# Kernel tuning notes

Hardware: AMD Instinct MI355X
Metric: run time of the kernel (lower is better)

The kernel has to match this reference:

```python
import jax, jax.numpy as jnp
import numpy as np

N_NODES = 50000
N_EDGES = 800000
D_NODE = 128
D_EDGE = 16
HID = 128
BN_EPS = 1e-5


def gcn_conv(h, src, dst, W, b):
    # PyG GCNConv: h' = D^-1/2 (A + I) D^-1/2 (h W) + b, deg includes self-loop
    h = h @ W
    deg = jax.ops.segment_sum(jnp.ones((src.shape[0],), h.dtype), dst,
                              num_segments=N_NODES) + 1.0
    dinv = deg ** -0.5
    norm = dinv[src] * dinv[dst]                      # [E]
    agg = jax.ops.segment_sum(h[src] * norm[:, None], dst,
                              num_segments=N_NODES)   # scatter to dst
    agg = agg + h * (dinv * dinv)[:, None]            # self-loop term
    return agg + b


def setup_inputs() -> dict:
    key = jax.random.key(0)
    ks = jax.random.split(key, 12)
    s = lambda fan_in: 1.0 / np.sqrt(fan_in)
    return {
        "x": jax.random.normal(ks[0], (N_NODES, D_NODE), jnp.float32),
        "edge_index": jax.random.randint(ks[1], (2, N_EDGES), 0, N_NODES, jnp.int32),
        "edge_attr": jax.random.normal(ks[2], (N_EDGES, D_EDGE), jnp.float32),
        "W1": jax.random.normal(ks[3], (D_NODE, HID), jnp.float32) * s(D_NODE),
        "b1": jnp.zeros((HID,), jnp.float32),
        "gamma": jnp.ones((HID,), jnp.float32),
        "beta": jnp.zeros((HID,), jnp.float32),
        "W2": jax.random.normal(ks[4], (HID, HID), jnp.float32) * s(HID),
        "b2": jnp.zeros((HID,), jnp.float32),
        "Wm1": jax.random.normal(ks[5], (2 * HID + D_EDGE, HID), jnp.float32) * s(2 * HID + D_EDGE),
        "bm1": jnp.zeros((HID,), jnp.float32),
        "Wm2": jax.random.normal(ks[6], (HID, 1), jnp.float32) * s(HID),
        "bm2": jnp.zeros((1,), jnp.float32),
    }


def reference(x, edge_index, edge_attr, W1, b1, gamma, beta, W2, b2, Wm1, bm1, Wm2, bm2):
    src, dst = edge_index[0], edge_index[1]
    z = gcn_conv(x, src, dst, W1, b1)
    # BatchNorm1d over nodes (training-mode batch stats, biased var)
    mean = jnp.mean(z, axis=0)
    var = jnp.mean(jnp.square(z - mean), axis=0)
    z = (z - mean) * jax.lax.rsqrt(var + BN_EPS) * gamma + beta
    z = jax.nn.relu(z)
    z = gcn_conv(z, src, dst, W2, b2)
    # edge head: gather endpoints, concat with edge_attr, 2-layer MLP (dropout = eval identity)
    edge_input = jnp.concatenate([z[src], z[dst], edge_attr], axis=1)  # [E, 2H+De]
    h = jax.nn.relu(edge_input @ Wm1 + bm1)
    return (h @ Wm2 + bm2).squeeze(-1)  # [E]
```

## Files before the change

### kernel.cpp

```cpp
#include <hip/hip_runtime.h>
#include <hip/hip_bf16.h>

#define NN 50000
#define NE 800000
#define H 128
#define DE 16
#define BN_EPS 1e-5f
#define NB_SCAN 196
#define NB_E 3125

typedef float v2f __attribute__((ext_vector_type(2)));
typedef float v4f __attribute__((ext_vector_type(4)));
typedef short bfrag __attribute__((ext_vector_type(8)));

__device__ __forceinline__ unsigned int packbf2(float a, float b) {
    __hip_bfloat162 h = __float22bfloat162_rn(make_float2(a, b));
    return *(unsigned int*)&h;
}
__device__ __forceinline__ v2f unpackbf2(unsigned int u) {
    v2f r;
    r.x = __uint_as_float(u << 16);
    r.y = __uint_as_float(u & 0xffff0000u);
    return r;
}
__device__ __forceinline__ bfrag cvt8(float4 a0, float4 a1) {
    union { uint4 u; bfrag f; } x;
    x.u.x = packbf2(a0.x, a0.y);
    x.u.y = packbf2(a0.z, a0.w);
    x.u.z = packbf2(a1.x, a1.y);
    x.u.w = packbf2(a1.z, a1.w);
    return x.f;
}
__device__ __forceinline__ bfrag cvt8v(v4f a0, v4f a1) {
    union { uint4 u; bfrag f; } x;
    x.u.x = packbf2(a0.x, a0.y);
    x.u.y = packbf2(a0.z, a0.w);
    x.u.z = packbf2(a1.x, a1.y);
    x.u.w = packbf2(a1.z, a1.w);
    return x.f;
}
#define COMP(u4, j) ((j) == 0 ? (u4).x : (j) == 1 ? (u4).y : (j) == 2 ? (u4).z : (u4).w)

__device__ __forceinline__ float dpp_rowred16(float s) {
    s += __int_as_float(__builtin_amdgcn_update_dpp(0, __float_as_int(s), 0x121, 0xf, 0xf, false));
    s += __int_as_float(__builtin_amdgcn_update_dpp(0, __float_as_int(s), 0x122, 0xf, 0xf, false));
    s += __int_as_float(__builtin_amdgcn_update_dpp(0, __float_as_int(s), 0x124, 0xf, 0xf, false));
    s += __int_as_float(__builtin_amdgcn_update_dpp(0, __float_as_int(s), 0x128, 0xf, 0xf, false));
    return s;
}

__global__ __launch_bounds__(256) void histcvt_k(const int* __restrict__ dst,
                                                 int* __restrict__ counts,
                                                 const float* __restrict__ W1,
                                                 const float* __restrict__ W2,
                                                 const float* __restrict__ Ws,
                                                 const float* __restrict__ Wd,
                                                 const float* __restrict__ We,
                                                 short* __restrict__ d1, short* __restrict__ d2,
                                                 short* __restrict__ ds_, short* __restrict__ dd,
                                                 unsigned int* __restrict__ WePk) {
    int b = blockIdx.x;
    if (b < NB_E) {
        int e = b * 256 + threadIdx.x;
        atomicAdd(&counts[dst[e]], 1);
        return;
    }
    b -= NB_E;
    if (b < 256) {
        int mat = b >> 6;
        const float* s = mat == 0 ? W1 : mat == 1 ? W2 : mat == 2 ? Ws : Wd;
        short* d = mat == 0 ? d1 : mat == 1 ? d2 : mat == 2 ? ds_ : dd;
        int idx = (b & 63) * 256 + threadIdx.x;
        int n = idx & 127, k = idx >> 7;
        float v = s[k * 128 + n];
        d[n * 128 + k] = (short)(packbf2(v, v) & 0xffff);
    } else {
        int idx = (b - 256) * 256 + threadIdx.x;
        int c = idx >> 8;
        int lane = (idx >> 2) & 63;
        int j2 = (idx & 3) * 2;
        int q = lane >> 4, i = lane & 15;
        int k0 = q * 8 + j2, k1 = k0 + 1;
        int feat = i * 8 + c;
        float v0 = (k0 < 16) ? We[k0 * 128 + feat] : 0.f;
        float v1 = (k1 < 16) ? We[k1 * 128 + feat] : 0.f;
        WePk[idx] = packbf2(v0, v1);
    }
}

__global__ void scan1_k(const int* __restrict__ counts, int* __restrict__ bsum) {
    __shared__ int sh[256];
    int i = blockIdx.x * 256 + threadIdx.x;
    int v = (i < NN) ? counts[i] : 0;
    sh[threadIdx.x] = v;
    __syncthreads();
    for (int off = 128; off; off >>= 1) {
        if (threadIdx.x < off) sh[threadIdx.x] += sh[threadIdx.x + off];
        __syncthreads();
    }
    if (!threadIdx.x) bsum[blockIdx.x] = sh[0];
}

__global__ void scan23_k(const int* __restrict__ counts, const int* __restrict__ bsum,
                         int* __restrict__ offsets, int* __restrict__ cursor,
                         float* __restrict__ dinv) {
    __shared__ int bs[256];
    __shared__ int sh[256];
    int t = threadIdx.x;
    int bv = (t < NB_SCAN) ? bsum[t] : 0;
    bs[t] = bv;
    __syncthreads();
    for (int off = 1; off < 256; off <<= 1) {
        int x = (t >= off) ? bs[t - off] : 0;
        __syncthreads();
        bs[t] += x;
        __syncthreads();
    }
    int bexcl = (blockIdx.x > 0) ? bs[blockIdx.x - 1] : 0;
    int i = blockIdx.x * 256 + t;
    int v = (i < NN) ? counts[i] : 0;
    sh[t] = v;
    __syncthreads();
    for (int off = 1; off < 256; off <<= 1) {
        int x = (t >= off) ? sh[t - off] : 0;
        __syncthreads();
        sh[t] += x;
        __syncthreads();
    }
    if (i < NN) {
        int excl = sh[t] - v + bexcl;
        offsets[i] = excl;
        cursor[i] = excl;
        dinv[i] = rsqrtf((float)v + 1.0f);
    }
}

__global__ __launch_bounds__(256) void fillgemm_k(const int* __restrict__ src,
                                                  const int* __restrict__ dst,
                                                  int* __restrict__ cursor,
                                                  int* __restrict__ srcs,
                                                  const float* __restrict__ A,
                                                  const short* __restrict__ Bt,
                                                  unsigned int* __restrict__ Cb,
                                                  const float* __restrict__ rowScale) {
    if (blockIdx.x < NB_E) {
        int e = blockIdx.x * 256 + threadIdx.x;
        int d = dst[e];
        int pos = atomicAdd(&cursor[d], 1);
        srcs[pos] = src[e];
        return;
    }
    int bid = blockIdx.x - NB_E;
    int lane = threadIdx.x & 63;
    int w = threadIdx.x >> 6;
    int i = lane & 15;
    int q = lane >> 4;
    int r0 = bid * 64 + w * 16;
    int arow = min(r0 + i, NN - 1);
    const float* Arow = A + (size_t)arow * 128;

    v4f acc[8];
#pragma unroll
    for (int c = 0; c < 8; c++) acc[c] = (v4f)0.f;

#pragma unroll
    for (int kc = 0; kc < 128; kc += 32) {
        int kb = kc + q * 8;
        float4 a0 = *(const float4*)&Arow[kb];
        float4 a1 = *(const float4*)&Arow[kb + 4];
        bfrag af = cvt8(a0, a1);
#pragma unroll
        for (int c = 0; c < 8; c++) {
            bfrag bf = *(const bfrag*)&Bt[(size_t)(c * 16 + i) * 128 + kb];
            acc[c] = __builtin_amdgcn_mfma_f32_16x16x32_bf16(af, bf, acc[c], 0, 0, 0);
        }
    }

    int orow0 = r0 + q * 4;
    v4f ds = *(const v4f*)&rowScale[min(orow0, NN - 4)];
#pragma unroll
    for (int c = 0; c < 8; c++) {
        int col = c * 16 + i;
#pragma unroll
        for (int r = 0; r < 4; r++) {
            float v = acc[c][r] * ds[r];
            float vp = __shfl_xor(v, 1, 64);
            if (!(i & 1) && orow0 + r < NN)
                Cb[(size_t)(orow0 + r) * 64 + (col >> 1)] = packbf2(v, vp);
        }
    }
}

__global__ __launch_bounds__(256) void gemm_bn_k(const unsigned int* __restrict__ Ab,
                                                 const short* __restrict__ Bt,
                                                 unsigned int* __restrict__ Cb,
                                                 const float* __restrict__ rowScale,
                                                 const float* __restrict__ sums,
                                                 const float* __restrict__ sumsq,
                                                 const float* __restrict__ gamma,
                                                 const float* __restrict__ beta) {
    __shared__ __align__(16) float tAs[128], tCs[128];
    if (threadIdx.x < 128) {
        int f = threadIdx.x;
        float mean = sums[f] * (1.0f / NN);
        float var = sumsq[f] * (1.0f / NN) - mean * mean;
        float a = gamma[f] * rsqrtf(var + BN_EPS);
        tAs[f] = a;
        tCs[f] = beta[f] - mean * a;
    }
    __syncthreads();

    int lane = threadIdx.x & 63;
    int w = threadIdx.x >> 6;
    int i = lane & 15;
    int q = lane >> 4;
    int r0 = blockIdx.x * 64 + w * 16;
    int arow = min(r0 + i, NN - 1);

    v4f acc[8];
#pragma unroll
    for (int c = 0; c < 8; c++) acc[c] = (v4f)0.f;

#pragma unroll
    for (int kc = 0; kc < 128; kc += 32) {
        int kb = kc + q * 8;
        uint4 u = *(const uint4*)&Ab[(size_t)arow * 64 + (kb >> 1)];
        v2f z0 = unpackbf2(u.x), z1 = unpackbf2(u.y);
        v2f z2 = unpackbf2(u.z), z3 = unpackbf2(u.w);
        v2f t0 = *(const v2f*)&tAs[kb],     c0 = *(const v2f*)&tCs[kb];
        v2f t1 = *(const v2f*)&tAs[kb + 2], c1 = *(const v2f*)&tCs[kb + 2];
        v2f t2 = *(const v2f*)&tAs[kb + 4], c2 = *(const v2f*)&tCs[kb + 4];
        v2f t3 = *(const v2f*)&tAs[kb + 6], c3 = *(const v2f*)&tCs[kb + 6];
        z0 = z0 * t0 + c0; z1 = z1 * t1 + c1;
        z2 = z2 * t2 + c2; z3 = z3 * t3 + c3;
        union { uint4 u; bfrag f; } x;
        x.u.x = packbf2(fmaxf(z0.x, 0.f), fmaxf(z0.y, 0.f));
        x.u.y = packbf2(fmaxf(z1.x, 0.f), fmaxf(z1.y, 0.f));
        x.u.z = packbf2(fmaxf(z2.x, 0.f), fmaxf(z2.y, 0.f));
        x.u.w = packbf2(fmaxf(z3.x, 0.f), fmaxf(z3.y, 0.f));
        bfrag af = x.f;
#pragma unroll
        for (int c = 0; c < 8; c++) {
            bfrag bf = *(const bfrag*)&Bt[(size_t)(c * 16 + i) * 128 + kb];
            acc[c] = __builtin_amdgcn_mfma_f32_16x16x32_bf16(af, bf, acc[c], 0, 0, 0);
        }
    }

    int orow0 = r0 + q * 4;
    v4f ds = *(const v4f*)&rowScale[min(orow0, NN - 4)];
#pragma unroll
    for (int c = 0; c < 8; c++) {
        int col = c * 16 + i;
#pragma unroll
        for (int r = 0; r < 4; r++) {
            float v = acc[c][r] * ds[r];
            float vp = __shfl_xor(v, 1, 64);
            if (!(i & 1) && orow0 + r < NN)
                Cb[(size_t)(orow0 + r) * 64 + (col >> 1)] = packbf2(v, vp);
        }
    }
}

__global__ __launch_bounds__(256) void gemm_pq(const unsigned int* __restrict__ zbA,
                                               const short* __restrict__ Bs_,
                                               const short* __restrict__ Bd_,
                                               const float* __restrict__ bm1,
                                               unsigned int* __restrict__ Pb,
                                               unsigned int* __restrict__ Qb,
                                               int M) {
    int lane = threadIdx.x & 63;
    int w = threadIdx.x >> 6;
    int i = lane & 15;
    int q = lane >> 4;
    int r0 = blockIdx.x * 64 + w * 16;
    int arow = min(r0 + i, M - 1);

    v4f accP[8], accQ[8];
#pragma unroll
    for (int c = 0; c < 8; c++) { accP[c] = (v4f)0.f; accQ[c] = (v4f)0.f; }

#pragma unroll
    for (int kc = 0; kc < 128; kc += 32) {
        int kb = kc + q * 8;
        bfrag af = *(const bfrag*)&zbA[(size_t)arow * 64 + (kb >> 1)];
#pragma unroll
        for (int c = 0; c < 8; c++) {
            bfrag bs = *(const bfrag*)&Bs_[(size_t)(c * 16 + i) * 128 + kb];
            bfrag bd = *(const bfrag*)&Bd_[(size_t)(c * 16 + i) * 128 + kb];
            accP[c] = __builtin_amdgcn_mfma_f32_16x16x32_bf16(af, bs, accP[c], 0, 0, 0);
            accQ[c] = __builtin_amdgcn_mfma_f32_16x16x32_bf16(af, bd, accQ[c], 0, 0, 0);
        }
    }

    int orow0 = r0 + q * 4;
    float bm1c[8];
#pragma unroll
    for (int c = 0; c < 8; c++) bm1c[c] = bm1[c * 16 + i];
#pragma unroll
    for (int c = 0; c < 8; c++) {
        int col = c * 16 + i;
#pragma unroll
        for (int r = 0; r < 4; r++) {
            float vP = accP[c][r];
            float vPp = __shfl_xor(vP, 1, 64);
            float vQ = accQ[c][r] + bm1c[c];
            float vQp = __shfl_xor(vQ, 1, 64);
            if (!(i & 1) && orow0 + r < M) {
                Pb[(size_t)(orow0 + r) * 64 + (col >> 1)] = packbf2(vP, vPp);
                Qb[(size_t)(orow0 + r) * 64 + (col >> 1)] = packbf2(vQ, vQp);
            }
        }
    }
}

__global__ __launch_bounds__(256) void aggregate_k(const unsigned int* __restrict__ hsb,
                                                   const int* __restrict__ offsets,
                                                   const int* __restrict__ counts,
                                                   const int* __restrict__ srcs,
                                                   const float* __restrict__ dinv,
                                                   const float* __restrict__ bias,
                                                   unsigned int* __restrict__ zbout) {
    int lane = threadIdx.x & 63;
    int i = lane & 15;
    int q = lane >> 4;
    int n = __builtin_amdgcn_readfirstlane(blockIdx.x * 4 + (threadIdx.x >> 6));
    if (n >= NN) return;
    int beg = offsets[n];
    int cnt = counts[n];
    v2f A0 = {0.f, 0.f}, A1 = {0.f, 0.f}, A2 = {0.f, 0.f}, A3 = {0.f, 0.f};
    v2f B0 = {0.f, 0.f}, B1 = {0.f, 0.f}, B2 = {0.f, 0.f}, B3 = {0.f, 0.f};
    for (int c = 0; c < cnt; c += 64) {
        int vsrc = srcs[beg + c + lane];
        int m = min(64, cnt - c);
        int ngrp = m >> 2;
        int g = 0;
        for (; g + 4 <= ngrp; g += 4) {
            int s0 = __shfl(vsrc, g * 4 + q, 64);
            int s1 = __shfl(vsrc, g * 4 + 4 + q, 64);
            int s2 = __shfl(vsrc, g * 4 + 8 + q, 64);
            int s3 = __shfl(vsrc, g * 4 + 12 + q, 64);
            uint4 u0 = *(const uint4*)&hsb[(size_t)s0 * 64 + i * 4];
            uint4 u1 = *(const uint4*)&hsb[(size_t)s1 * 64 + i * 4];
            uint4 u2 = *(const uint4*)&hsb[(size_t)s2 * 64 + i * 4];
            uint4 u3 = *(const uint4*)&hsb[(size_t)s3 * 64 + i * 4];
            A0 += unpackbf2(u0.x); A1 += unpackbf2(u0.y); A2 += unpackbf2(u0.z); A3 += unpackbf2(u0.w);
            B0 += unpackbf2(u1.x); B1 += unpackbf2(u1.y); B2 += unpackbf2(u1.z); B3 += unpackbf2(u1.w);
            A0 += unpackbf2(u2.x); A1 += unpackbf2(u2.y); A2 += unpackbf2(u2.z); A3 += unpackbf2(u2.w);
            B0 += unpackbf2(u3.x); B1 += unpackbf2(u3.y); B2 += unpackbf2(u3.z); B3 += unpackbf2(u3.w);
        }
        for (; g < ngrp; g++) {
            int s0 = __shfl(vsrc, g * 4 + q, 64);
            uint4 u0 = *(const uint4*)&hsb[(size_t)s0 * 64 + i * 4];
            A0 += unpackbf2(u0.x); A1 += unpackbf2(u0.y); A2 += unpackbf2(u0.z); A3 += unpackbf2(u0.w);
        }
        int rem = m & 3;
        if (rem) {
            int s0 = __shfl(vsrc, (m & ~3) + q, 64);
            if (q < rem) {
                uint4 u0 = *(const uint4*)&hsb[(size_t)s0 * 64 + i * 4];
                B0 += unpackbf2(u0.x); B1 += unpackbf2(u0.y); B2 += unpackbf2(u0.z); B3 += unpackbf2(u0.w);
            }
        }
    }
    A0 += B0; A1 += B1; A2 += B2; A3 += B3;
    A0.x += __shfl_xor(A0.x, 32, 64); A0.y += __shfl_xor(A0.y, 32, 64);
    A1.x += __shfl_xor(A1.x, 32, 64); A1.y += __shfl_xor(A1.y, 32, 64);
    A2.x += __shfl_xor(A2.x, 32, 64); A2.y += __shfl_xor(A2.y, 32, 64);
    A3.x += __shfl_xor(A3.x, 32, 64); A3.y += __shfl_xor(A3.y, 32, 64);
    bool hi = (lane & 32) != 0;
    v2f U0, U1;
    U0.x = hi ? A2.x : A0.x; U0.y = hi ? A2.y : A0.y;
    U1.x = hi ? A3.x : A1.x; U1.y = hi ? A3.y : A1.y;
    U0.x += __shfl_xor(U0.x, 16, 64); U0.y += __shfl_xor(U0.y, 16, 64);
    U1.x += __shfl_xor(U1.x, 16, 64); U1.y += __shfl_xor(U1.y, 16, 64);
    bool lo = (lane & 16) != 0;
    v2f res;
    res.x = lo ? U1.x : U0.x;
    res.y = lo ? U1.y : U0.y;
    int ui = i * 4 + q;
    v2f self = unpackbf2(hsb[(size_t)n * 64 + ui]);
    float di = dinv[n];
    float2 b = *(const float2*)&bias[ui * 2];
    float rx = (res.x + self.x) * di + b.x;
    float ry = (res.y + self.y) * di + b.y;
    zbout[(size_t)n * 64 + ui] = packbf2(rx, ry);
}

__global__ __launch_bounds__(256) void bnstats_b_k(const unsigned int* __restrict__ zb,
                                                   float* __restrict__ sums,
                                                   float* __restrict__ sumsq) {
    __shared__ v2f ls[4][64], lq[4][64];
    int lane = threadIdx.x & 63;
    int sub = threadIdx.x >> 6;
    v2f s = {0.f, 0.f}, q = {0.f, 0.f};
    for (int r = blockIdx.x * 4 + sub; r < NN; r += gridDim.x * 4) {
        v2f v = unpackbf2(zb[(size_t)r * 64 + lane]);
        s += v;
        q += v * v;
    }
    if (sub) { ls[sub][lane] = s; lq[sub][lane] = q; }
    __syncthreads();
    if (!sub) {
        s += ls[1][lane] + ls[2][lane] + ls[3][lane];
        q += lq[1][lane] + lq[2][lane] + lq[3][lane];
        atomicAdd(&sums[lane * 2], s.x);
        atomicAdd(&sums[lane * 2 + 1], s.y);
        atomicAdd(&sumsq[lane * 2], q.x);
        atomicAdd(&sumsq[lane * 2 + 1], q.y);
    }
}

__global__ __launch_bounds__(256) void edgehead_k(const unsigned int* __restrict__ Pb,
                                                  const unsigned int* __restrict__ Qb,
                                                  const float* __restrict__ ea,
                                                  const int* __restrict__ srcI,
                                                  const int* __restrict__ dstI,
                                                  const unsigned int* __restrict__ WePk,
                                                  const float* __restrict__ Wm2,
                                                  const float* __restrict__ bm2,
                                                  float* __restrict__ out) {
    int lane = threadIdx.x & 63;
    int wid = threadIdx.x >> 6;
    int base = (blockIdx.x * 4 + wid) * 64;
    int i = lane & 15;
    int q = lane >> 4;

    bfrag wef[8];
#pragma unroll
    for (int c = 0; c < 8; c++)
        wef[c] = *(const bfrag*)&WePk[(c * 64 + lane) * 4];
    float4 wv0 = *(const float4*)&Wm2[i * 8];
    float4 wv1 = *(const float4*)&Wm2[i * 8 + 4];
    v2f wv2[4];
    wv2[0].x = wv0.x; wv2[0].y = wv0.y;
    wv2[1].x = wv0.z; wv2[1].y = wv0.w;
    wv2[2].x = wv1.x; wv2[2].y = wv1.y;
    wv2[3].x = wv1.z; wv2[3].y = wv1.w;
    float bm2v = bm2[0];

    int sv = srcI[base + lane];
    int dv = dstI[base + lane];

#pragma unroll
    for (int t = 0; t < 4; t++) {
        int tb = t * 16;
        bfrag af;
#pragma unroll
        for (int z = 0; z < 8; z++) af[z] = 0;
        if (q < 2) {
            const float* erow = &ea[(size_t)(base + tb + i) * 16 + q * 8];
            v4f e0 = __builtin_nontemporal_load((const v4f*)erow);
            v4f e1 = __builtin_nontemporal_load((const v4f*)(erow + 4));
            af = cvt8v(e0, e1);
        }
        uint4 Pu[4], Qu[4];
#pragma unroll
        for (int r = 0; r < 4; r++) {
            int sr = __shfl(sv, tb + q * 4 + r, 64);
            int dr = __shfl(dv, tb + q * 4 + r, 64);
            Pu[r] = *(const uint4*)&Pb[(size_t)sr * 64 + i * 4];
            Qu[r] = *(const uint4*)&Qb[(size_t)dr * 64 + i * 4];
        }
        v4f acc[8];
#pragma unroll
        for (int c = 0; c < 8; c++) acc[c] = (v4f)0.f;
#pragma unroll
        for (int c = 0; c < 8; c++)
            acc[c] = __builtin_amdgcn_mfma_f32_16x16x32_bf16(af, wef[c], acc[c], 0, 0, 0);
#pragma unroll
        for (int r = 0; r < 4; r++) {
            v2f sa = {0.f, 0.f};
#pragma unroll
            for (int j = 0; j < 4; j++) {
                v2f pq = unpackbf2(COMP(Pu[r], j)) + unpackbf2(COMP(Qu[r], j));
                v2f tt;
                tt.x = acc[2 * j][r] + pq.x;
                tt.y = acc[2 * j + 1][r] + pq.y;
                tt.x = fmaxf(tt.x, 0.f);
                tt.y = fmaxf(tt.y, 0.f);
                sa += tt * wv2[j];
            }
            float s = dpp_rowred16(sa.x + sa.y);
            if (i == 0) __builtin_nontemporal_store(s + bm2v, &out[base + tb + q * 4 + r]);
        }
    }
}

extern "C" void kernel_launch(void* const* d_in, const int* in_sizes, int n_in,
                              void* d_out, int out_size, void* d_ws, size_t ws_size,
                              hipStream_t stream) {
    const float* x     = (const float*)d_in[0];
    const int*   ei    = (const int*)d_in[1];
    const float* ea    = (const float*)d_in[2];
    const float* W1    = (const float*)d_in[3];
    const float* b1    = (const float*)d_in[4];
    const float* gamma = (const float*)d_in[5];
    const float* beta  = (const float*)d_in[6];
    const float* W2    = (const float*)d_in[7];
    const float* b2    = (const float*)d_in[8];
    const float* Wm1   = (const float*)d_in[9];
    const float* bm1   = (const float*)d_in[10];
    const float* Wm2   = (const float*)d_in[11];
    const float* bm2   = (const float*)d_in[12];
    float* out = (float*)d_out;

    const int* srcI = ei;
    const int* dstI = ei + NE;

    char* w = (char*)d_ws;
    auto alloc = [&](size_t bytes) {
        char* p = w;
        w += (bytes + 255) & ~(size_t)255;
        return p;
    };
    int*   counts  = (int*)alloc((NN + 256) * 4);
    float* sums    = (float*)(counts + NN);
    float* sumsq   = sums + 128;
    float* dinv    = (float*)alloc(NN * 4);
    int*   offsets = (int*)alloc(NN * 4);
    int*   cursor  = (int*)alloc(NN * 4);
    int*   bsum    = (int*)alloc(256 * 4);
    int*   srcs    = (int*)alloc((size_t)(NE + 64) * 4);
    short* bt1     = (short*)alloc(128 * 128 * 2);
    short* bt2     = (short*)alloc(128 * 128 * 2);
    short* bts     = (short*)alloc(128 * 128 * 2);
    short* btd     = (short*)alloc(128 * 128 * 2);
    unsigned int* WePk = (unsigned int*)alloc(2048 * 4);
    unsigned int* hsb  = (unsigned int*)alloc((size_t)NN * 64 * 4);
    unsigned int* zb1  = (unsigned int*)alloc((size_t)NN * 64 * 4);
    unsigned int* Qb   = (unsigned int*)alloc((size_t)NN * 64 * 4);
    unsigned int* zb2  = zb1;

    hipMemsetAsync(counts, 0, (NN + 256) * 4, stream);

    histcvt_k<<<NB_E + 264, 256, 0, stream>>>(dstI, counts, W1, W2, Wm1,
                                              Wm1 + 128 * 128, Wm1 + 256 * 128,
                                              bt1, bt2, bts, btd, WePk);
    scan1_k<<<NB_SCAN, 256, 0, stream>>>(counts, bsum);
    scan23_k<<<NB_SCAN, 256, 0, stream>>>(counts, bsum, offsets, cursor, dinv);

    const int GB = (NN + 63) / 64;
    const int AGG = (NN + 3) / 4;

    fillgemm_k<<<NB_E + GB, 256, 0, stream>>>(srcI, dstI, cursor, srcs,
                                              x, bt1, hsb, dinv);
    aggregate_k<<<AGG, 256, 0, stream>>>(hsb, offsets, counts, srcs, dinv, b1, zb1);
    bnstats_b_k<<<256, 256, 0, stream>>>(zb1, sums, sumsq);
    gemm_bn_k<<<GB, 256, 0, stream>>>(zb1, bt2, hsb, dinv, sums, sumsq, gamma, beta);
    aggregate_k<<<AGG, 256, 0, stream>>>(hsb, offsets, counts, srcs, dinv, b2, zb2);
    gemm_pq<<<GB, 256, 0, stream>>>(zb2, bts, btd, bm1, hsb, Qb, NN);
    edgehead_k<<<NB_E, 256, 0, stream>>>(hsb, Qb, ea, srcI, dstI, WePk,
                                         Wm2, bm2, out);
}
```

Baseline: 447.9 us.

## Replace global counting sort of edges with two-level bucketed CSR build

Edges are first scattered into coarse buckets of 256 destination nodes, split into sub-buckets, using a packed src and local-dst word. A per-bucket kernel then builds the histogram, prefix offsets, degree normalisation and the sorted source list entirely with shared-memory atomics. This removes the scattered global atomics on per-node counters and cursors, and replaces the two-kernel global scan with a single small bucket scan. The first GEMM now runs as its own launch instead of being fused with the fill. The fixed sub-bucket capacity and 16-bit source packing assume bounded bucket sizes and fewer than 65536 nodes.

New measurement: 509.1 us. +13.7%, slower.

```diff
diff --git a/kernel.cpp b/kernel.cpp
--- a/kernel.cpp
+++ b/kernel.cpp
@@ -6,8 +6,10 @@
 #define H 128
 #define DE 16
 #define BN_EPS 1e-5f
-#define NB_SCAN 196
 #define NB_E 3125
+#define NBKT 196
+#define NSUB 8
+#define BCAP 768
 
 typedef float v2f __attribute__((ext_vector_type(2)));
 typedef float v4f __attribute__((ext_vector_type(4)));
@@ -49,20 +51,26 @@
     return s;
 }
 
-__global__ __launch_bounds__(256) void histcvt_k(const int* __restrict__ dst,
-                                                 int* __restrict__ counts,
-                                                 const float* __restrict__ W1,
-                                                 const float* __restrict__ W2,
-                                                 const float* __restrict__ Ws,
-                                                 const float* __restrict__ Wd,
-                                                 const float* __restrict__ We,
-                                                 short* __restrict__ d1, short* __restrict__ d2,
-                                                 short* __restrict__ ds_, short* __restrict__ dd,
-                                                 unsigned int* __restrict__ WePk) {
+__global__ __launch_bounds__(256) void bucketcvt_k(const int* __restrict__ src,
+                                                   const int* __restrict__ dst,
+                                                   int* __restrict__ bcur,
+                                                   unsigned int* __restrict__ tmp,
+                                                   const float* __restrict__ W1,
+                                                   const float* __restrict__ W2,
+                                                   const float* __restrict__ Ws,
+                                                   const float* __restrict__ Wd,
+                                                   const float* __restrict__ We,
+                                                   short* __restrict__ d1, short* __restrict__ d2,
+                                                   short* __restrict__ ds_, short* __restrict__ dd,
+                                                   unsigned int* __restrict__ WePk) {
     int b = blockIdx.x;
     if (b < NB_E) {
         int e = b * 256 + threadIdx.x;
-        atomicAdd(&counts[dst[e]], 1);
+        int d = dst[e];
+        int s = src[e];
+        int sb = (d >> 8) * NSUB + (b & (NSUB - 1));
+        int pos = atomicAdd(&bcur[sb], 1);
+        tmp[(size_t)sb * BCAP + pos] = (unsigned int)s | ((unsigned int)(d & 255) << 16);
         return;
     }
     b -= NB_E;
@@ -88,74 +96,86 @@
     }
 }
 
-__global__ void scan1_k(const int* __restrict__ counts, int* __restrict__ bsum) {
-    __shared__ int sh[256];
-    int i = blockIdx.x * 256 + threadIdx.x;
-    int v = (i < NN) ? counts[i] : 0;
-    sh[threadIdx.x] = v;
-    __syncthreads();
-    for (int off = 128; off; off >>= 1) {
-        if (threadIdx.x < off) sh[threadIdx.x] += sh[threadIdx.x + off];
-        __syncthreads();
-    }
-    if (!threadIdx.x) bsum[blockIdx.x] = sh[0];
-}
-
-__global__ void scan23_k(const int* __restrict__ counts, const int* __restrict__ bsum,
-                         int* __restrict__ offsets, int* __restrict__ cursor,
-                         float* __restrict__ dinv) {
-    __shared__ int bs[256];
+__global__ void bscan_k(const int* __restrict__ bcur, int* __restrict__ bbase) {
     __shared__ int sh[256];
     int t = threadIdx.x;
-    int bv = (t < NB_SCAN) ? bsum[t] : 0;
-    bs[t] = bv;
+    int tot = 0;
+    if (t < NBKT) {
+#pragma unroll
+        for (int x = 0; x < NSUB; x++) tot += bcur[t * NSUB + x];
+    }
+    sh[t] = tot;
     __syncthreads();
     for (int off = 1; off < 256; off <<= 1) {
-        int x = (t >= off) ? bs[t - off] : 0;
+        int v = (t >= off) ? sh[t - off] : 0;
         __syncthreads();
-        bs[t] += x;
+        sh[t] += v;
         __syncthreads();
     }
-    int bexcl = (blockIdx.x > 0) ? bs[blockIdx.x - 1] : 0;
-    int i = blockIdx.x * 256 + t;
-    int v = (i < NN) ? counts[i] : 0;
-    sh[t] = v;
-    __syncthreads();
-    for (int off = 1; off < 256; off <<= 1) {
-        int x = (t >= off) ? sh[t - off] : 0;
+    if (t < NBKT) bbase[t] = sh[t] - tot;
+}
+
+__global__ __launch_bounds__(256) void fillb_k(const int* __restrict__ bcur,
+                                               const int* __restrict__ bbase,
+                                               const unsigned int* __restrict__ tmp,
+                                               int* __restrict__ counts,
+                                               int* __restrict__ offsets,
+                                               float* __restrict__ dinv,
+                                               int* __restrict__ srcs) {
+    __shared__ int hist[256], off[256];
+    int t = threadIdx.x;
+    int b = blockIdx.x;
+    hist[t] = 0;
+    __syncthreads();
+    int base = bbase[b];
+#pragma unroll
+    for (int x = 0; x < NSUB; x++) {
+        int nbx = bcur[b * NSUB + x];
+        const unsigned int* tp = tmp + (size_t)(b * NSUB + x) * BCAP;
+        for (int idx = t; idx < nbx; idx += 256)
+            atomicAdd(&hist[tp[idx] >> 16], 1);
+    }
+    __syncthreads();
+    int h = hist[t];
+    off[t] = h;
+    __syncthreads();
+    for (int o = 1; o < 256; o <<= 1) {
+        int v = (t >= o) ? off[t - o] : 0;
         __syncthreads();
-        sh[t] += x;
+        off[t] += v;
         __syncthreads();
     }
-    if (i < NN) {
-        int excl = sh[t] - v + bexcl;
-        offsets[i] = excl;
-        cursor[i] = excl;
-        dinv[i] = rsqrtf((float)v + 1.0f);
-    }
-}
-
-__global__ __launch_bounds__(256) void fillgemm_k(const int* __restrict__ src,
-                                                  const int* __restrict__ dst,
-                                                  int* __restrict__ cursor,
-                                                  int* __restrict__ srcs,
-                                                  const float* __restrict__ A,
-                                                  const short* __restrict__ Bt,
-                                                  unsigned int* __restrict__ Cb,
-                                                  const float* __restrict__ rowScale) {
-    if (blockIdx.x < NB_E) {
-        int e = blockIdx.x * 256 + threadIdx.x;
-        int d = dst[e];
-        int pos = atomicAdd(&cursor[d], 1);
-        srcs[pos] = src[e];
-        return;
-    }
-    int bid = blockIdx.x - NB_E;
+    int excl = off[t] - h;
+    int node = b * 256 + t;
+    if (node < NN) {
+        counts[node] = h;
+        offsets[node] = base + excl;
+        dinv[node] = rsqrtf((float)h + 1.0f);
+    }
+    __syncthreads();
+    hist[t] = excl;
+    __syncthreads();
+#pragma unroll
+    for (int x = 0; x < NSUB; x++) {
+        int nbx = bcur[b * NSUB + x];
+        const unsigned int* tp = tmp + (size_t)(b * NSUB + x) * BCAP;
+        for (int idx = t; idx < nbx; idx += 256) {
+            unsigned int u = tp[idx];
+            int pos = atomicAdd(&hist[u >> 16], 1);
+            srcs[base + pos] = (int)(u & 0xffffu);
+        }
+    }
+}
+
+__global__ __launch_bounds__(256) void gemm1_k(const float* __restrict__ A,
+                                               const short* __restrict__ Bt,
+                                               unsigned int* __restrict__ Cb,
+                                               const float* __restrict__ rowScale) {
     int lane = threadIdx.x & 63;
     int w = threadIdx.x >> 6;
     int i = lane & 15;
     int q = lane >> 4;
-    int r0 = bid * 64 + w * 16;
+    int r0 = blockIdx.x * 64 + w * 16;
     int arow = min(r0 + i, NN - 1);
     const float* Arow = A + (size_t)arow * 128;
 
@@ -513,13 +533,14 @@
         w += (bytes + 255) & ~(size_t)255;
         return p;
     };
-    int*   counts  = (int*)alloc((NN + 256) * 4);
-    float* sums    = (float*)(counts + NN);
+    int*   bcur    = (int*)alloc((NBKT * NSUB + 256) * 4);
+    float* sums    = (float*)(bcur + NBKT * NSUB);
     float* sumsq   = sums + 128;
+    int*   bbase   = (int*)alloc(NBKT * 4);
+    unsigned int* tmp = (unsigned int*)alloc((size_t)NBKT * NSUB * BCAP * 4);
+    int*   counts  = (int*)alloc(NN * 4);
+    int*   offsets = (int*)alloc(NN * 4);
     float* dinv    = (float*)alloc(NN * 4);
-    int*   offsets = (int*)alloc(NN * 4);
-    int*   cursor  = (int*)alloc(NN * 4);
-    int*   bsum    = (int*)alloc(256 * 4);
     int*   srcs    = (int*)alloc((size_t)(NE + 64) * 4);
     short* bt1     = (short*)alloc(128 * 128 * 2);
     short* bt2     = (short*)alloc(128 * 128 * 2);
@@ -531,19 +552,19 @@
     unsigned int* Qb   = (unsigned int*)alloc((size_t)NN * 64 * 4);
     unsigned int* zb2  = zb1;
 
-    hipMemsetAsync(counts, 0, (NN + 256) * 4, stream);
-
-    histcvt_k<<<NB_E + 264, 256, 0, stream>>>(dstI, counts, W1, W2, Wm1,
-                                              Wm1 + 128 * 128, Wm1 + 256 * 128,
-                                              bt1, bt2, bts, btd, WePk);
-    scan1_k<<<NB_SCAN, 256, 0, stream>>>(counts, bsum);
-    scan23_k<<<NB_SCAN, 256, 0, stream>>>(counts, bsum, offsets, cursor, dinv);
+    hipMemsetAsync(bcur, 0, (NBKT * NSUB + 256) * 4, stream);
+
+    bucketcvt_k<<<NB_E + 264, 256, 0, stream>>>(srcI, dstI, bcur, tmp,
+                                                W1, W2, Wm1, Wm1 + 128 * 128,
+                                                Wm1 + 256 * 128,
+                                                bt1, bt2, bts, btd, WePk);
+    bscan_k<<<1, 256, 0, stream>>>(bcur, bbase);
+    fillb_k<<<NBKT, 256, 0, stream>>>(bcur, bbase, tmp, counts, offsets, dinv, srcs);
 
     const int GB = (NN + 63) / 64;
     const int AGG = (NN + 3) / 4;
 
-    fillgemm_k<<<NB_E + GB, 256, 0, stream>>>(srcI, dstI, cursor, srcs,
-                                              x, bt1, hsb, dinv);
+    gemm1_k<<<GB, 256, 0, stream>>>(x, bt1, hsb, dinv);
     aggregate_k<<<AGG, 256, 0, stream>>>(hsb, offsets, counts, srcs, dinv, b1, zb1);
     bnstats_b_k<<<256, 256, 0, stream>>>(zb1, sums, sumsq);
     gemm_bn_k<<<GB, 256, 0, stream>>>(zb1, bt2, hsb, dinv, sums, sumsq, gamma, beta);
```
